# Kernel tuning notes

Measured on AMD Instinct MI355X. Metric: run time of the kernel, lower is better.

The kernel has to match this reference:

```python
import jax, jax.numpy as jnp
import numpy as np

N_NODES = 50000


def _sage_conv(x, src, dst, Wl, Wr, b):
    """SAGEConv with mean aggregation: lin_l(mean_j x_j) + lin_r(x_i) + b."""
    msgs = x[src]                                                # [E, Din] gather
    agg = jax.ops.segment_sum(msgs, dst, num_segments=N_NODES)  # [N, Din] scatter-add
    cnt = jax.ops.segment_sum(jnp.ones((src.shape[0], 1), x.dtype), dst,
                              num_segments=N_NODES)             # [N, 1]
    agg = agg / jnp.maximum(cnt, 1.0)                           # mean
    return agg @ Wl.T + x @ Wr.T + b                            # [N, Dout]


def setup_inputs() -> dict:
    key = jax.random.key(0)
    ks = jax.random.split(key, 8)
    d_in, d_h = 64, 128
    x = jax.random.normal(ks[0], (N_NODES, d_in), dtype=jnp.float32)
    edge_index = jax.random.randint(ks[1], (2, 800000), 0, N_NODES, dtype=jnp.int32)
    s1 = 1.0 / np.sqrt(d_in)
    s2 = 1.0 / np.sqrt(d_h)
    return {
        "x": x,
        "edge_index": edge_index,
        "Wl1": jax.random.normal(ks[2], (d_h, d_in), dtype=jnp.float32) * s1,
        "Wr1": jax.random.normal(ks[3], (d_h, d_in), dtype=jnp.float32) * s1,
        "b1": jnp.zeros((d_h,), dtype=jnp.float32),
        "Wl2": jax.random.normal(ks[4], (d_h, d_h), dtype=jnp.float32) * s2,
        "Wr2": jax.random.normal(ks[5], (d_h, d_h), dtype=jnp.float32) * s2,
        "b2": jnp.zeros((d_h,), dtype=jnp.float32),
    }


def reference(x, edge_index, Wl1, Wr1, b1, Wl2, Wr2, b2):
    src, dst = edge_index[0], edge_index[1]
    # layer 1: conv -> dropout(eval: identity) -> ReLU
    h = jax.nn.relu(_sage_conv(x, src, dst, Wl1, Wr1, b1))
    # layer 2
    h = jax.nn.relu(_sage_conv(h, src, dst, Wl2, Wr2, b2))
    return h
```

## Files before the change

### kernel.cpp

```cpp
#include <hip/hip_runtime.h>

#define N_NODES 50000
#define NBUCK 782
#define BCAP 2048
#define BSHIFT 11

typedef __attribute__((ext_vector_type(8))) short short8;
typedef __attribute__((ext_vector_type(4))) float floatx4;
typedef __attribute__((ext_vector_type(2))) float floatx2;
typedef __attribute__((ext_vector_type(2))) int intx2;

static __device__ __forceinline__ unsigned short f2bf(float f) {
  unsigned int u = __builtin_bit_cast(unsigned int, f);
  u += 0x7fff + ((u >> 16) & 1);
  return (unsigned short)(u >> 16);
}
static __device__ __forceinline__ void fp8x8_acc(intx2 v, floatx2* ac) {
  ac[0] += __builtin_amdgcn_cvt_pk_f32_fp8(v[0], false);
  ac[1] += __builtin_amdgcn_cvt_pk_f32_fp8(v[0], true);
  ac[2] += __builtin_amdgcn_cvt_pk_f32_fp8(v[1], false);
  ac[3] += __builtin_amdgcn_cvt_pk_f32_fp8(v[1], true);
}


__global__ void __launch_bounds__(512) prep_scatter(
    const float* __restrict__ x,
    const float* __restrict__ Wl1, const float* __restrict__ Wr1,
    const float* __restrict__ Wl2, const float* __restrict__ Wr2,
    unsigned short* __restrict__ xb, unsigned char* __restrict__ xq,
    unsigned short* __restrict__ W1, unsigned short* __restrict__ W2,
    const int* __restrict__ src, const int* __restrict__ dst,
    int* __restrict__ bucket_cur, int* __restrict__ buf, int E, int n) {
  const int t = threadIdx.x;
  const int gid = blockIdx.x * 512 + t;
  const int gsz = gridDim.x * 512;
  for (int i = gid; i < n * 16; i += gsz) {
    float4 v = ((const float4*)x)[i];
    unsigned int lo = (unsigned int)f2bf(v.x) | ((unsigned int)f2bf(v.y) << 16);
    unsigned int hi = (unsigned int)f2bf(v.z) | ((unsigned int)f2bf(v.w) << 16);
    ((uint2*)xb)[i] = make_uint2(lo, hi);
    int q = __builtin_amdgcn_cvt_pk_fp8_f32(v.x, v.y, 0, false);
    q = __builtin_amdgcn_cvt_pk_fp8_f32(v.z, v.w, q, true);
    ((int*)xq)[i] = q;
  }
  {
    unsigned char* h1q = xq + ((size_t)n + 1) * 64;
    if (gid < 16) ((int*)(xq + (size_t)n * 64))[gid] = 0;
    if (gid >= 16 && gid < 48) ((int*)(h1q + (size_t)n * 128))[gid - 16] = 0;
  }
  for (int i = gid; i < 128 * 128; i += gsz) {
    int c = i >> 7, k = i & 127;
    W1[i] = f2bf(k < 64 ? Wl1[c * 64 + k] : Wr1[c * 64 + k - 64]);
  }
  for (int i = gid; i < 128 * 256; i += gsz) {
    int c = i >> 8, k = i & 255;
    W2[i] = f2bf(k < 128 ? Wl2[c * 128 + k] : Wr2[c * 128 + k - 128]);
  }

  __shared__ int hist[NBUCK];
  __shared__ int base_s[NBUCK];
  for (int i = t; i < NBUCK; i += 512) hist[i] = 0;
  __syncthreads();
  int e0 = blockIdx.x * 4096;
  int sv[8], dv[8], bv[8];
#pragma unroll
  for (int p = 0; p < 8; ++p) {
    int e = e0 + p * 512 + t;
    if (e < E) {
      sv[p] = src[e];
      dv[p] = dst[e];
      bv[p] = dv[p] >> 6;
      atomicAdd(&hist[bv[p]], 1);
    } else bv[p] = -1;
  }
  __syncthreads();
  for (int i = t; i < NBUCK; i += 512) {
    int c = hist[i];
    base_s[i] = c > 0 ? atomicAdd(&bucket_cur[i], c) : 0;
  }
  __syncthreads();
  for (int i = t; i < NBUCK; i += 512) hist[i] = 0;
  __syncthreads();
#pragma unroll
  for (int p = 0; p < 8; ++p) {
    if (bv[p] >= 0) {
      int sub = base_s[bv[p]] + atomicAdd(&hist[bv[p]], 1);
      if (sub < BCAP) buf[(bv[p] << BSHIFT) + sub] = (sv[p] << 6) | (dv[p] & 63);
    }
  }
}


__global__ void __launch_bounds__(512, 6) csr_agg_gemm1(
    int* __restrict__ buf, const int* __restrict__ bucket_cur,
    int* __restrict__ row_start, int* __restrict__ row_cnt,
    const unsigned short* __restrict__ xb, const unsigned char* __restrict__ xq,
    const unsigned short* __restrict__ W1, const float* __restrict__ b1,
    unsigned short* __restrict__ h1, unsigned char* __restrict__ h1q, int n) {
  __shared__ int eb[BCAP];
  __shared__ int gsrc[BCAP];
  __shared__ __align__(16) unsigned short aggS[64 * 72];
  __shared__ int cnt[64];
  __shared__ int tmp[64];
  __shared__ int cur[64];
  const int t = threadIdx.x;
  const int b = blockIdx.x;
  const int node0 = b << 6;
  const int len = min(bucket_cur[b], BCAP);
  int* reg = buf + (b << BSHIFT);

  if (t < 64) cnt[t] = 0;
  __syncthreads();
  for (int i = t; i < len; i += 512) {
    int p = reg[i];
    eb[i] = p;
    atomicAdd(&cnt[p & 63], 1);
  }
  __syncthreads();
  if (t < 64) tmp[t] = (cnt[t] + 7) & ~7;
  __syncthreads();
#pragma unroll
  for (int off = 1; off < 64; off <<= 1) {
    int u = (t >= off && t < 64) ? tmp[t - off] : 0;
    __syncthreads();
    if (t < 64) tmp[t] += u;
    __syncthreads();
  }
  if (t < 64) {
    int c8 = (cnt[t] + 7) & ~7;
    int ex = tmp[t] - c8;
    cur[t] = ex;
    int nd = node0 + t;
    if (nd < n) {
      row_start[nd] = (b << BSHIFT) + ex;
      row_cnt[nd] = cnt[t];
    }
  }
  __syncthreads();
  for (int i = t; i < len; i += 512) {
    int p = eb[i];
    int sub = atomicAdd(&cur[p & 63], 1);
    int s = p >> 6;
    if (sub < BCAP) { gsrc[sub] = s; reg[sub] = s; }
  }
  __syncthreads();
  if (t < 64) {
    int c8 = (cnt[t] + 7) & ~7;
    int e1 = tmp[t];
    for (int j = e1 - c8 + cnt[t]; j < e1; ++j)
      if (j < BCAP) { gsrc[j] = n; reg[j] = n; }
  }
  __syncthreads();

  const int lane = t & 63;
  const int wv = t >> 6;
  const int eq = lane >> 3;
  const int cl = lane & 7;
#pragma unroll 1
  for (int p = 0; p < 4; ++p) {
    int locA = wv + p * 16;
    int locB = locA + 8;
    int cnA = cnt[locA], cnB = cnt[locB];
    int cpA = (cnA + 7) & ~7, cpB = (cnB + 7) & ~7;
    int baseA = tmp[locA] - cpA;
    int baseB = tmp[locB] - cpB;
    floatx2 aA[4], aB[4];
#pragma unroll
    for (int j = 0; j < 4; ++j) { aA[j] = (floatx2){0.f, 0.f}; aB[j] = (floatx2){0.f, 0.f}; }
    int mx = max(cpA, cpB);
    int sA = (0 < cpA) ? gsrc[baseA + eq] : n;
    int sB = (0 < cpB) ? gsrc[baseB + eq] : n;
    int sA1 = (8 < cpA) ? gsrc[baseA + 8 + eq] : n;
    int sB1 = (8 < cpB) ? gsrc[baseB + 8 + eq] : n;
    intx2 vA = *(const intx2*)(xq + (size_t)sA * 64 + cl * 8);
    intx2 vB = *(const intx2*)(xq + (size_t)sB * 64 + cl * 8);
    intx2 uA = *(const intx2*)(xq + (size_t)sA1 * 64 + cl * 8);
    intx2 uB = *(const intx2*)(xq + (size_t)sB1 * 64 + cl * 8);
    for (int e = 16; e < mx; e += 8) {
      int nA = (e < cpA) ? gsrc[baseA + e + eq] : n;
      int nB = (e < cpB) ? gsrc[baseB + e + eq] : n;
      intx2 wA = *(const intx2*)(xq + (size_t)nA * 64 + cl * 8);
      intx2 wB = *(const intx2*)(xq + (size_t)nB * 64 + cl * 8);
      fp8x8_acc(vA, aA);
      fp8x8_acc(vB, aB);
      vA = uA; vB = uB; uA = wA; uB = wB;
    }
    fp8x8_acc(vA, aA);
    fp8x8_acc(vB, aB);
    fp8x8_acc(uA, aA);
    fp8x8_acc(uB, aB);
    float rA[8], rB[8];
#pragma unroll
    for (int j = 0; j < 4; ++j) {
      rA[2 * j] = aA[j][0]; rA[2 * j + 1] = aA[j][1];
      rB[2 * j] = aB[j][0]; rB[2 * j + 1] = aB[j][1];
    }
#pragma unroll
    for (int j = 0; j < 8; ++j) {
      rA[j] += __shfl_xor(rA[j], 8, 64);
      rA[j] += __shfl_xor(rA[j], 16, 64);
      rA[j] += __shfl_xor(rA[j], 32, 64);
      rB[j] += __shfl_xor(rB[j], 8, 64);
      rB[j] += __shfl_xor(rB[j], 16, 64);
      rB[j] += __shfl_xor(rB[j], 32, 64);
    }
    if (eq == 0) {
      float invA = 1.0f / (float)max(cnA, 1);
      float invB = 1.0f / (float)max(cnB, 1);
      short8 oA, oB;
#pragma unroll
      for (int j = 0; j < 8; ++j) { oA[j] = (short)f2bf(rA[j] * invA); oB[j] = (short)f2bf(rB[j] * invB); }
      *(short8*)(aggS + locA * 72 + cl * 8) = oA;
      *(short8*)(aggS + locB * 72 + cl * 8) = oB;
    }
  }
  __syncthreads();

  const int m = lane & 15;
  const int q = lane >> 4;
  const int rw = (wv & 1) * 32;
  const int cw = (wv >> 1) * 32;
  floatx4 acc[2][2];
#pragma unroll
  for (int rt = 0; rt < 2; ++rt)
#pragma unroll
    for (int ct = 0; ct < 2; ++ct) acc[rt][ct] = (floatx4){0.f, 0.f, 0.f, 0.f};

  int ra = node0 + rw + m;      if (ra > n - 1) ra = n - 1;
  int rb = node0 + rw + 16 + m; if (rb > n - 1) rb = n - 1;
  const unsigned short* selfA0 = xb + (size_t)ra * 64 + q * 8;
  const unsigned short* selfA1 = xb + (size_t)rb * 64 + q * 8;
  const unsigned short* aggL0 = aggS + (rw + m) * 72 + q * 8;
  const unsigned short* aggL1 = aggS + (rw + 16 + m) * 72 + q * 8;
  const unsigned short* Wc0 = W1 + (size_t)(cw + m) * 128 + q * 8;
  const unsigned short* Wc1 = W1 + (size_t)(cw + 16 + m) * 128 + q * 8;

#pragma unroll
  for (int kc = 0; kc < 2; ++kc) {
    short8 a0 = *(const short8*)(aggL0 + kc * 32);
    short8 a1 = *(const short8*)(aggL1 + kc * 32);
    short8 w0 = *(const short8*)(Wc0 + kc * 32);
    short8 w1 = *(const short8*)(Wc1 + kc * 32);
    acc[0][0] = __builtin_amdgcn_mfma_f32_16x16x32_bf16(a0, w0, acc[0][0], 0, 0, 0);
    acc[0][1] = __builtin_amdgcn_mfma_f32_16x16x32_bf16(a0, w1, acc[0][1], 0, 0, 0);
    acc[1][0] = __builtin_amdgcn_mfma_f32_16x16x32_bf16(a1, w0, acc[1][0], 0, 0, 0);
    acc[1][1] = __builtin_amdgcn_mfma_f32_16x16x32_bf16(a1, w1, acc[1][1], 0, 0, 0);
  }
#pragma unroll
  for (int kc = 0; kc < 2; ++kc) {
    short8 a0 = *(const short8*)(selfA0 + kc * 32);
    short8 a1 = *(const short8*)(selfA1 + kc * 32);
    short8 w0 = *(const short8*)(Wc0 + 64 + kc * 32);
    short8 w1 = *(const short8*)(Wc1 + 64 + kc * 32);
    acc[0][0] = __builtin_amdgcn_mfma_f32_16x16x32_bf16(a0, w0, acc[0][0], 0, 0, 0);
    acc[0][1] = __builtin_amdgcn_mfma_f32_16x16x32_bf16(a0, w1, acc[0][1], 0, 0, 0);
    acc[1][0] = __builtin_amdgcn_mfma_f32_16x16x32_bf16(a1, w0, acc[1][0], 0, 0, 0);
    acc[1][1] = __builtin_amdgcn_mfma_f32_16x16x32_bf16(a1, w1, acc[1][1], 0, 0, 0);
  }

  float bv0 = b1[cw + m], bv1 = b1[cw + 16 + m];
#pragma unroll
  for (int rt = 0; rt < 2; ++rt) {
#pragma unroll
    for (int j = 0; j < 4; ++j) {
      int row = node0 + rw + rt * 16 + q * 4 + j;
      if (row < n) {
        float v0 = acc[rt][0][j] + bv0; v0 = v0 > 0.f ? v0 : 0.f;
        float v1 = acc[rt][1][j] + bv1; v1 = v1 > 0.f ? v1 : 0.f;
        h1[(size_t)row * 128 + cw + m] = f2bf(v0);
        h1[(size_t)row * 128 + cw + 16 + m] = f2bf(v1);
        h1q[(size_t)row * 128 + cw + m] =
            (unsigned char)__builtin_amdgcn_cvt_pk_fp8_f32(v0, v0, 0, false);
        h1q[(size_t)row * 128 + cw + 16 + m] =
            (unsigned char)__builtin_amdgcn_cvt_pk_fp8_f32(v1, v1, 0, false);
      }
    }
  }
}


__global__ void __launch_bounds__(512, 6) agg_gemm2(
    const unsigned short* __restrict__ h1, const unsigned char* __restrict__ h1q,
    const int* __restrict__ row_start, const int* __restrict__ row_cnt,
    const int* __restrict__ buf, const unsigned short* __restrict__ W2,
    const float* __restrict__ b2, float* __restrict__ out, int n) {
  __shared__ int gsrcS[BCAP];
  __shared__ __align__(16) unsigned short aggS[64 * 136];
  __shared__ int cntS[64];
  __shared__ int stS[64];
  const int t = threadIdx.x;
  const int lane = t & 63;
  const int wv = t >> 6;
  const int node0 = blockIdx.x << 6;
  const int boff = blockIdx.x << BSHIFT;

  {
    const int4* b4 = (const int4*)(buf + ((size_t)blockIdx.x << BSHIFT));
    ((int4*)gsrcS)[t] = b4[t];
  }
  if (t < 64) {
    int nd = node0 + t;
    cntS[t] = (nd < n) ? row_cnt[nd] : 0;
    stS[t]  = (nd < n) ? (row_start[nd] - boff) : 0;
  }
  __syncthreads();

  const int eq = lane >> 4;
  const int cl = lane & 15;
#pragma unroll 1
  for (int lp = 0; lp < 4; ++lp) {
    int locA = wv + lp * 16;
    int locB = locA + 8;
    int cnA = cntS[locA], stA = stS[locA];
    int cnB = cntS[locB], stB = stS[locB];
    int cpA = (cnA + 7) & ~7, cpB = (cnB + 7) & ~7;
    int mx = max(cpA, cpB);
    floatx2 aA[4], aB[4];
#pragma unroll
    for (int j = 0; j < 4; ++j) { aA[j] = (floatx2){0.f, 0.f}; aB[j] = (floatx2){0.f, 0.f}; }
    int iA0 = (0 < cpA) ? gsrcS[stA + eq] : n;
    int iA1 = (0 < cpA) ? gsrcS[stA + 4 + eq] : n;
    int iB0 = (0 < cpB) ? gsrcS[stB + eq] : n;
    int iB1 = (0 < cpB) ? gsrcS[stB + 4 + eq] : n;
    intx2 vA0 = *(const intx2*)(h1q + (size_t)iA0 * 128 + cl * 8);
    intx2 vA1 = *(const intx2*)(h1q + (size_t)iA1 * 128 + cl * 8);
    intx2 vB0 = *(const intx2*)(h1q + (size_t)iB0 * 128 + cl * 8);
    intx2 vB1 = *(const intx2*)(h1q + (size_t)iB1 * 128 + cl * 8);
    int jA0 = (8 < cpA) ? gsrcS[stA + 8 + eq] : n;
    int jA1 = (8 < cpA) ? gsrcS[stA + 12 + eq] : n;
    int jB0 = (8 < cpB) ? gsrcS[stB + 8 + eq] : n;
    int jB1 = (8 < cpB) ? gsrcS[stB + 12 + eq] : n;
    intx2 uA0 = *(const intx2*)(h1q + (size_t)jA0 * 128 + cl * 8);
    intx2 uA1 = *(const intx2*)(h1q + (size_t)jA1 * 128 + cl * 8);
    intx2 uB0 = *(const intx2*)(h1q + (size_t)jB0 * 128 + cl * 8);
    intx2 uB1 = *(const intx2*)(h1q + (size_t)jB1 * 128 + cl * 8);
    for (int e = 16; e < mx; e += 8) {
      int kA0 = (e < cpA) ? gsrcS[stA + e + eq] : n;
      int kA1 = (e < cpA) ? gsrcS[stA + e + 4 + eq] : n;
      int kB0 = (e < cpB) ? gsrcS[stB + e + eq] : n;
      int kB1 = (e < cpB) ? gsrcS[stB + e + 4 + eq] : n;
      intx2 wA0 = *(const intx2*)(h1q + (size_t)kA0 * 128 + cl * 8);
      intx2 wA1 = *(const intx2*)(h1q + (size_t)kA1 * 128 + cl * 8);
      intx2 wB0 = *(const intx2*)(h1q + (size_t)kB0 * 128 + cl * 8);
      intx2 wB1 = *(const intx2*)(h1q + (size_t)kB1 * 128 + cl * 8);
      fp8x8_acc(vA0, aA); fp8x8_acc(vA1, aA);
      fp8x8_acc(vB0, aB); fp8x8_acc(vB1, aB);
      vA0 = uA0; vA1 = uA1; vB0 = uB0; vB1 = uB1;
      uA0 = wA0; uA1 = wA1; uB0 = wB0; uB1 = wB1;
    }
    fp8x8_acc(vA0, aA); fp8x8_acc(vA1, aA);
    fp8x8_acc(vB0, aB); fp8x8_acc(vB1, aB);
    fp8x8_acc(uA0, aA); fp8x8_acc(uA1, aA);
    fp8x8_acc(uB0, aB); fp8x8_acc(uB1, aB);

    float rA[8], rB[8];
#pragma unroll
    for (int j = 0; j < 4; ++j) {
      rA[2 * j] = aA[j][0]; rA[2 * j + 1] = aA[j][1];
      rB[2 * j] = aB[j][0]; rB[2 * j + 1] = aB[j][1];
    }
#pragma unroll
    for (int j = 0; j < 8; ++j) {
      rA[j] += __shfl_xor(rA[j], 16, 64);
      rA[j] += __shfl_xor(rA[j], 32, 64);
      rB[j] += __shfl_xor(rB[j], 16, 64);
      rB[j] += __shfl_xor(rB[j], 32, 64);
    }
    if (eq == 0) {
      float invA = 1.0f / (float)max(cnA, 1);
      float invB = 1.0f / (float)max(cnB, 1);
      short8 oA, oB;
#pragma unroll
      for (int j = 0; j < 8; ++j) { oA[j] = (short)f2bf(rA[j] * invA); oB[j] = (short)f2bf(rB[j] * invB); }
      *(short8*)(aggS + locA * 136 + cl * 8) = oA;
      *(short8*)(aggS + locB * 136 + cl * 8) = oB;
    }
  }
  __syncthreads();

  const int m = lane & 15;
  const int q = lane >> 4;
  const int rw = (wv & 1) * 32;
  const int cw = (wv >> 1) * 32;
  floatx4 acc[2][2];
#pragma unroll
  for (int rt = 0; rt < 2; ++rt)
#pragma unroll
    for (int ct = 0; ct < 2; ++ct) acc[rt][ct] = (floatx4){0.f, 0.f, 0.f, 0.f};

  int ra = node0 + rw + m;      if (ra > n - 1) ra = n - 1;
  int rb = node0 + rw + 16 + m; if (rb > n - 1) rb = n - 1;
  const unsigned short* selfA0 = h1 + (size_t)ra * 128 + q * 8;
  const unsigned short* selfA1 = h1 + (size_t)rb * 128 + q * 8;
  const unsigned short* aggL0 = aggS + (rw + m) * 136 + q * 8;
  const unsigned short* aggL1 = aggS + (rw + 16 + m) * 136 + q * 8;
  const unsigned short* Wc0 = W2 + (size_t)(cw + m) * 256 + q * 8;
  const unsigned short* Wc1 = W2 + (size_t)(cw + 16 + m) * 256 + q * 8;

#pragma unroll
  for (int kc = 0; kc < 4; ++kc) {
    short8 a0 = *(const short8*)(aggL0 + kc * 32);
    short8 a1 = *(const short8*)(aggL1 + kc * 32);
    short8 w0 = *(const short8*)(Wc0 + kc * 32);
    short8 w1 = *(const short8*)(Wc1 + kc * 32);
    acc[0][0] = __builtin_amdgcn_mfma_f32_16x16x32_bf16(a0, w0, acc[0][0], 0, 0, 0);
    acc[0][1] = __builtin_amdgcn_mfma_f32_16x16x32_bf16(a0, w1, acc[0][1], 0, 0, 0);
    acc[1][0] = __builtin_amdgcn_mfma_f32_16x16x32_bf16(a1, w0, acc[1][0], 0, 0, 0);
    acc[1][1] = __builtin_amdgcn_mfma_f32_16x16x32_bf16(a1, w1, acc[1][1], 0, 0, 0);
  }
#pragma unroll
  for (int kc = 0; kc < 4; ++kc) {
    short8 a0 = *(const short8*)(selfA0 + kc * 32);
    short8 a1 = *(const short8*)(selfA1 + kc * 32);
    short8 w0 = *(const short8*)(Wc0 + 128 + kc * 32);
    short8 w1 = *(const short8*)(Wc1 + 128 + kc * 32);
    acc[0][0] = __builtin_amdgcn_mfma_f32_16x16x32_bf16(a0, w0, acc[0][0], 0, 0, 0);
    acc[0][1] = __builtin_amdgcn_mfma_f32_16x16x32_bf16(a0, w1, acc[0][1], 0, 0, 0);
    acc[1][0] = __builtin_amdgcn_mfma_f32_16x16x32_bf16(a1, w0, acc[1][0], 0, 0, 0);
    acc[1][1] = __builtin_amdgcn_mfma_f32_16x16x32_bf16(a1, w1, acc[1][1], 0, 0, 0);
  }

  float bv0 = b2[cw + m], bv1 = b2[cw + 16 + m];
#pragma unroll
  for (int rt = 0; rt < 2; ++rt) {
#pragma unroll
    for (int j = 0; j < 4; ++j) {
      int row = node0 + rw + rt * 16 + q * 4 + j;
      if (row < n) {
        float v0 = acc[rt][0][j] + bv0; v0 = v0 > 0.f ? v0 : 0.f;
        float v1 = acc[rt][1][j] + bv1; v1 = v1 > 0.f ? v1 : 0.f;
        out[(size_t)row * 128 + cw + m] = v0;
        out[(size_t)row * 128 + cw + 16 + m] = v1;
      }
    }
  }
}


extern "C" void kernel_launch(void* const* d_in, const int* in_sizes, int n_in,
                              void* d_out, int out_size, void* d_ws, size_t ws_size,
                              hipStream_t stream) {
  const int N = N_NODES;
  const int E = in_sizes[1] / 2;
  const float* x   = (const float*)d_in[0];
  const int*   src = (const int*)d_in[1];
  const int*   dst = src + E;
  const float* Wl1 = (const float*)d_in[2];
  const float* Wr1 = (const float*)d_in[3];
  const float* b1  = (const float*)d_in[4];
  const float* Wl2 = (const float*)d_in[5];
  const float* Wr2 = (const float*)d_in[6];
  const float* b2  = (const float*)d_in[7];
  float* out = (float*)d_out;

  unsigned short* xb = (unsigned short*)d_ws;
  unsigned short* h1 = xb + (size_t)N * 64;
  unsigned short* W1 = h1 + (size_t)N * 128;
  unsigned short* W2 = W1 + 128 * 128;
  int* row_start  = (int*)(W2 + 128 * 256);
  int* row_cnt    = row_start + N;
  int* bucket_cur = row_cnt + N;
  int* buf        = bucket_cur + 784;
  unsigned char* xq  = (unsigned char*)(buf + (size_t)NBUCK * BCAP);
  unsigned char* h1q = xq + ((size_t)N + 1) * 64;

  (void)hipMemsetAsync(bucket_cur, 0, NBUCK * sizeof(int), stream);
  int sb = (E + 4095) / 4096;
  prep_scatter<<<sb, 512, 0, stream>>>(x, Wl1, Wr1, Wl2, Wr2, xb, xq, W1, W2,
                                       src, dst, bucket_cur, buf, E, N);
  csr_agg_gemm1<<<NBUCK, 512, 0, stream>>>(buf, bucket_cur, row_start, row_cnt,
                                           xb, xq, W1, b1, h1, h1q, N);
  agg_gemm2<<<NBUCK, 512, 0, stream>>>(h1, h1q, row_start, row_cnt, buf, W2, b2, out, N);
}
```

Before: 181.7 us.

## Split fp8 layer-1 features into two 64-column halves for gather locality

Stores the fp8 copy of the layer-1 hidden features as two separate 64-byte-per-row arrays (low and high column halves) instead of one 128-byte row array. The layer-2 aggregation then runs two passes, one per half, each gathering 64-byte rows with 8 lanes per row and 8 edges in flight. The aim is a smaller working set per pass (about 3.2 MB per half) so the random gathers hit cache more often. The cost is twice the loop and reduction work, an extra shuffle stage, and edge indices read twice.

```diff
diff --git a/kernel.cpp b/kernel.cpp
--- a/kernel.cpp
+++ b/kernel.cpp
@@ -29,6 +29,7 @@
     const float* __restrict__ Wl2, const float* __restrict__ Wr2,
     unsigned short* __restrict__ xb, unsigned char* __restrict__ xq,
     unsigned short* __restrict__ W1, unsigned short* __restrict__ W2,
+    unsigned char* __restrict__ h1q_lo, unsigned char* __restrict__ h1q_hi,
     const int* __restrict__ src, const int* __restrict__ dst,
     int* __restrict__ bucket_cur, int* __restrict__ buf, int E, int n) {
   const int t = threadIdx.x;
@@ -43,11 +44,9 @@
     q = __builtin_amdgcn_cvt_pk_fp8_f32(v.z, v.w, q, true);
     ((int*)xq)[i] = q;
   }
-  {
-    unsigned char* h1q = xq + ((size_t)n + 1) * 64;
-    if (gid < 16) ((int*)(xq + (size_t)n * 64))[gid] = 0;
-    if (gid >= 16 && gid < 48) ((int*)(h1q + (size_t)n * 128))[gid - 16] = 0;
-  }
+  if (gid < 16) ((int*)(xq + (size_t)n * 64))[gid] = 0;
+  if (gid >= 16 && gid < 32) ((int*)(h1q_lo + (size_t)n * 64))[gid - 16] = 0;
+  if (gid >= 32 && gid < 48) ((int*)(h1q_hi + (size_t)n * 64))[gid - 32] = 0;
   for (int i = gid; i < 128 * 128; i += gsz) {
     int c = i >> 7, k = i & 127;
     W1[i] = f2bf(k < 64 ? Wl1[c * 64 + k] : Wr1[c * 64 + k - 64]);
@@ -96,7 +95,8 @@
     int* __restrict__ row_start, int* __restrict__ row_cnt,
     const unsigned short* __restrict__ xb, const unsigned char* __restrict__ xq,
     const unsigned short* __restrict__ W1, const float* __restrict__ b1,
-    unsigned short* __restrict__ h1, unsigned char* __restrict__ h1q, int n) {
+    unsigned short* __restrict__ h1,
+    unsigned char* __restrict__ h1q_lo, unsigned char* __restrict__ h1q_hi, int n) {
   __shared__ int eb[BCAP];
   __shared__ int gsrc[BCAP];
   __shared__ __align__(16) unsigned short aggS[64 * 72];
@@ -259,6 +259,8 @@
   }
 
   float bv0 = b1[cw + m], bv1 = b1[cw + 16 + m];
+  unsigned char* hq = (cw < 64) ? h1q_lo : h1q_hi;
+  const int cbase = cw & 63;
 #pragma unroll
   for (int rt = 0; rt < 2; ++rt) {
 #pragma unroll
@@ -269,9 +271,9 @@
         float v1 = acc[rt][1][j] + bv1; v1 = v1 > 0.f ? v1 : 0.f;
         h1[(size_t)row * 128 + cw + m] = f2bf(v0);
         h1[(size_t)row * 128 + cw + 16 + m] = f2bf(v1);
-        h1q[(size_t)row * 128 + cw + m] =
+        hq[(size_t)row * 64 + cbase + m] =
             (unsigned char)__builtin_amdgcn_cvt_pk_fp8_f32(v0, v0, 0, false);
-        h1q[(size_t)row * 128 + cw + 16 + m] =
+        hq[(size_t)row * 64 + cbase + 16 + m] =
             (unsigned char)__builtin_amdgcn_cvt_pk_fp8_f32(v1, v1, 0, false);
       }
     }
@@ -280,7 +282,8 @@
 
 
 __global__ void __launch_bounds__(512, 6) agg_gemm2(
-    const unsigned short* __restrict__ h1, const unsigned char* __restrict__ h1q,
+    const unsigned short* __restrict__ h1,
+    const unsigned char* __restrict__ h1q_lo, const unsigned char* __restrict__ h1q_hi,
     const int* __restrict__ row_start, const int* __restrict__ row_cnt,
     const int* __restrict__ buf, const unsigned short* __restrict__ W2,
     const float* __restrict__ b2, float* __restrict__ out, int n) {
@@ -305,75 +308,67 @@
   }
   __syncthreads();
 
-  const int eq = lane >> 4;
-  const int cl = lane & 15;
+  const int eq = lane >> 3;
+  const int cl = lane & 7;
 #pragma unroll 1
-  for (int lp = 0; lp < 4; ++lp) {
-    int locA = wv + lp * 16;
-    int locB = locA + 8;
-    int cnA = cntS[locA], stA = stS[locA];
-    int cnB = cntS[locB], stB = stS[locB];
-    int cpA = (cnA + 7) & ~7, cpB = (cnB + 7) & ~7;
-    int mx = max(cpA, cpB);
-    floatx2 aA[4], aB[4];
-#pragma unroll
-    for (int j = 0; j < 4; ++j) { aA[j] = (floatx2){0.f, 0.f}; aB[j] = (floatx2){0.f, 0.f}; }
-    int iA0 = (0 < cpA) ? gsrcS[stA + eq] : n;
-    int iA1 = (0 < cpA) ? gsrcS[stA + 4 + eq] : n;
-    int iB0 = (0 < cpB) ? gsrcS[stB + eq] : n;
-    int iB1 = (0 < cpB) ? gsrcS[stB + 4 + eq] : n;
-    intx2 vA0 = *(const intx2*)(h1q + (size_t)iA0 * 128 + cl * 8);
-    intx2 vA1 = *(const intx2*)(h1q + (size_t)iA1 * 128 + cl * 8);
-    intx2 vB0 = *(const intx2*)(h1q + (size_t)iB0 * 128 + cl * 8);
-    intx2 vB1 = *(const intx2*)(h1q + (size_t)iB1 * 128 + cl * 8);
-    int jA0 = (8 < cpA) ? gsrcS[stA + 8 + eq] : n;
-    int jA1 = (8 < cpA) ? gsrcS[stA + 12 + eq] : n;
-    int jB0 = (8 < cpB) ? gsrcS[stB + 8 + eq] : n;
-    int jB1 = (8 < cpB) ? gsrcS[stB + 12 + eq] : n;
-    intx2 uA0 = *(const intx2*)(h1q + (size_t)jA0 * 128 + cl * 8);
-    intx2 uA1 = *(const intx2*)(h1q + (size_t)jA1 * 128 + cl * 8);
-    intx2 uB0 = *(const intx2*)(h1q + (size_t)jB0 * 128 + cl * 8);
-    intx2 uB1 = *(const intx2*)(h1q + (size_t)jB1 * 128 + cl * 8);
-    for (int e = 16; e < mx; e += 8) {
-      int kA0 = (e < cpA) ? gsrcS[stA + e + eq] : n;
-      int kA1 = (e < cpA) ? gsrcS[stA + e + 4 + eq] : n;
-      int kB0 = (e < cpB) ? gsrcS[stB + e + eq] : n;
-      int kB1 = (e < cpB) ? gsrcS[stB + e + 4 + eq] : n;
-      intx2 wA0 = *(const intx2*)(h1q + (size_t)kA0 * 128 + cl * 8);
-      intx2 wA1 = *(const intx2*)(h1q + (size_t)kA1 * 128 + cl * 8);
-      intx2 wB0 = *(const intx2*)(h1q + (size_t)kB0 * 128 + cl * 8);
-      intx2 wB1 = *(const intx2*)(h1q + (size_t)kB1 * 128 + cl * 8);
-      fp8x8_acc(vA0, aA); fp8x8_acc(vA1, aA);
-      fp8x8_acc(vB0, aB); fp8x8_acc(vB1, aB);
-      vA0 = uA0; vA1 = uA1; vB0 = uB0; vB1 = uB1;
-      uA0 = wA0; uA1 = wA1; uB0 = wB0; uB1 = wB1;
-    }
-    fp8x8_acc(vA0, aA); fp8x8_acc(vA1, aA);
-    fp8x8_acc(vB0, aB); fp8x8_acc(vB1, aB);
-    fp8x8_acc(uA0, aA); fp8x8_acc(uA1, aA);
-    fp8x8_acc(uB0, aB); fp8x8_acc(uB1, aB);
-
-    float rA[8], rB[8];
-#pragma unroll
-    for (int j = 0; j < 4; ++j) {
-      rA[2 * j] = aA[j][0]; rA[2 * j + 1] = aA[j][1];
-      rB[2 * j] = aB[j][0]; rB[2 * j + 1] = aB[j][1];
-    }
-#pragma unroll
-    for (int j = 0; j < 8; ++j) {
-      rA[j] += __shfl_xor(rA[j], 16, 64);
-      rA[j] += __shfl_xor(rA[j], 32, 64);
-      rB[j] += __shfl_xor(rB[j], 16, 64);
-      rB[j] += __shfl_xor(rB[j], 32, 64);
-    }
-    if (eq == 0) {
-      float invA = 1.0f / (float)max(cnA, 1);
-      float invB = 1.0f / (float)max(cnB, 1);
-      short8 oA, oB;
-#pragma unroll
-      for (int j = 0; j < 8; ++j) { oA[j] = (short)f2bf(rA[j] * invA); oB[j] = (short)f2bf(rB[j] * invB); }
-      *(short8*)(aggS + locA * 136 + cl * 8) = oA;
-      *(short8*)(aggS + locB * 136 + cl * 8) = oB;
+  for (int hp = 0; hp < 2; ++hp) {
+    const unsigned char* hq = hp ? h1q_hi : h1q_lo;
+#pragma unroll 1
+    for (int lp = 0; lp < 4; ++lp) {
+      int locA = wv + lp * 16;
+      int locB = locA + 8;
+      int cnA = cntS[locA], stA = stS[locA];
+      int cnB = cntS[locB], stB = stS[locB];
+      int cpA = (cnA + 7) & ~7, cpB = (cnB + 7) & ~7;
+      int mx = max(cpA, cpB);
+      floatx2 aA[4], aB[4];
+#pragma unroll
+      for (int j = 0; j < 4; ++j) { aA[j] = (floatx2){0.f, 0.f}; aB[j] = (floatx2){0.f, 0.f}; }
+      int sA = (0 < cpA) ? gsrcS[stA + eq] : n;
+      int sB = (0 < cpB) ? gsrcS[stB + eq] : n;
+      int sA1 = (8 < cpA) ? gsrcS[stA + 8 + eq] : n;
+      int sB1 = (8 < cpB) ? gsrcS[stB + 8 + eq] : n;
+      intx2 vA = *(const intx2*)(hq + (size_t)sA * 64 + cl * 8);
+      intx2 vB = *(const intx2*)(hq + (size_t)sB * 64 + cl * 8);
+      intx2 uA = *(const intx2*)(hq + (size_t)sA1 * 64 + cl * 8);
+      intx2 uB = *(const intx2*)(hq + (size_t)sB1 * 64 + cl * 8);
+      for (int e = 16; e < mx; e += 8) {
+        int nA = (e < cpA) ? gsrcS[stA + e + eq] : n;
+        int nB = (e < cpB) ? gsrcS[stB + e + eq] : n;
+        intx2 wA = *(const intx2*)(hq + (size_t)nA * 64 + cl * 8);
+        intx2 wB = *(const intx2*)(hq + (size_t)nB * 64 + cl * 8);
+        fp8x8_acc(vA, aA);
+        fp8x8_acc(vB, aB);
+        vA = uA; vB = uB; uA = wA; uB = wB;
+      }
+      fp8x8_acc(vA, aA);
+      fp8x8_acc(vB, aB);
+      fp8x8_acc(uA, aA);
+      fp8x8_acc(uB, aB);
+      float rA[8], rB[8];
+#pragma unroll
+      for (int j = 0; j < 4; ++j) {
+        rA[2 * j] = aA[j][0]; rA[2 * j + 1] = aA[j][1];
+        rB[2 * j] = aB[j][0]; rB[2 * j + 1] = aB[j][1];
+      }
+#pragma unroll
+      for (int j = 0; j < 8; ++j) {
+        rA[j] += __shfl_xor(rA[j], 8, 64);
+        rA[j] += __shfl_xor(rA[j], 16, 64);
+        rA[j] += __shfl_xor(rA[j], 32, 64);
+        rB[j] += __shfl_xor(rB[j], 8, 64);
+        rB[j] += __shfl_xor(rB[j], 16, 64);
+        rB[j] += __shfl_xor(rB[j], 32, 64);
+      }
+      if (eq == 0) {
+        float invA = 1.0f / (float)max(cnA, 1);
+        float invB = 1.0f / (float)max(cnB, 1);
+        short8 oA, oB;
+#pragma unroll
+        for (int j = 0; j < 8; ++j) { oA[j] = (short)f2bf(rA[j] * invA); oB[j] = (short)f2bf(rB[j] * invB); }
+        *(short8*)(aggS + locA * 136 + hp * 64 + cl * 8) = oA;
+        *(short8*)(aggS + locB * 136 + hp * 64 + cl * 8) = oB;
+      }
     }
   }
   __syncthreads();
@@ -461,14 +456,16 @@
   int* row_cnt    = row_start + N;
   int* bucket_cur = row_cnt + N;
   int* buf        = bucket_cur + 784;
-  unsigned char* xq  = (unsigned char*)(buf + (size_t)NBUCK * BCAP);
-  unsigned char* h1q = xq + ((size_t)N + 1) * 64;
+  unsigned char* xq     = (unsigned char*)(buf + (size_t)NBUCK * BCAP);
+  unsigned char* h1q_lo = xq + ((size_t)N + 1) * 64;
+  unsigned char* h1q_hi = h1q_lo + ((size_t)N + 1) * 64;
 
   (void)hipMemsetAsync(bucket_cur, 0, NBUCK * sizeof(int), stream);
   int sb = (E + 4095) / 4096;
   prep_scatter<<<sb, 512, 0, stream>>>(x, Wl1, Wr1, Wl2, Wr2, xb, xq, W1, W2,
-                                       src, dst, bucket_cur, buf, E, N);
+                                       h1q_lo, h1q_hi, src, dst, bucket_cur, buf, E, N);
   csr_agg_gemm1<<<NBUCK, 512, 0, stream>>>(buf, bucket_cur, row_start, row_cnt,
-                                           xb, xq, W1, b1, h1, h1q, N);
-  agg_gemm2<<<NBUCK, 512, 0, stream>>>(h1, h1q, row_start, row_cnt, buf, W2, b2, out, N);
-}
+                                           xb, xq, W1, b1, h1, h1q_lo, h1q_hi, N);
+  agg_gemm2<<<NBUCK, 512, 0, stream>>>(h1, h1q_lo, h1q_hi, row_start, row_cnt,
+                                       buf, W2, b2, out, N);
+}
```

Measured after the change: 192.7 us. 1.06x slower.
